# Performance work log

Hardware: AMD Instinct MI355X
Metric: run time of the kernel (lower is better)

## Reference

```python
import jax, jax.numpy as jnp
import numpy as np

NTOKEN, NINP, NHID = 50257, 256, 256
B, T = 64, 2048
RES, FC1 = 10, NHID // 3
EPS = 1e-5

def lrelu(x, p=0.01):
    return jnp.maximum(x, x * p)

def setup_inputs() -> dict:
    key = jax.random.key(0)
    ks = jax.random.split(key, 12)
    s = 0.05
    inp = {
        "input": jax.random.randint(ks[0], (B, T), 0, NTOKEN),
        "hx": jnp.zeros((B, NHID), jnp.float32),
        "cx": jnp.zeros((B, NHID), jnp.float32),
        "seq_len": jax.random.randint(ks[1], (B,), 1, T + 1),  # lengths in [1, T]
        "emb_w": jax.random.uniform(ks[2], (NTOKEN, NINP), jnp.float32, -0.1, 0.1),
        "W_ih": jax.random.normal(ks[3], (4 * NHID, NINP), jnp.float32) * s,
        "W_hh": jax.random.normal(ks[4], (4 * NHID, NHID), jnp.float32) * s,
        "b_ih": jnp.zeros((4 * NHID,), jnp.float32),
        "b_hh": jnp.zeros((4 * NHID,), jnp.float32),
        "rfc1_w": jax.random.normal(ks[5], (RES, NHID), jnp.float32) * s,
        "rfc1_b": jnp.zeros((RES,), jnp.float32),
        "rbn_g": jnp.ones((RES,), jnp.float32),
        "rbn_b": jnp.zeros((RES,), jnp.float32),
        "rbn_rm": jnp.zeros((RES,), jnp.float32),
        "rbn_rv": jnp.ones((RES,), jnp.float32),
        "rfc2_w": jax.random.normal(ks[6], (NHID, RES), jnp.float32) * s,
        "rfc2_b": jnp.zeros((NHID,), jnp.float32),
        "fc1_w": jax.random.normal(ks[7], (FC1, NHID), jnp.float32) * s,
        "fc1_b": jnp.zeros((FC1,), jnp.float32),
        "bn1_g": jnp.ones((FC1,), jnp.float32),
        "bn1_b": jnp.zeros((FC1,), jnp.float32),
        "bn1_rm": jnp.zeros((FC1,), jnp.float32),
        "bn1_rv": jnp.ones((FC1,), jnp.float32),
        "fc2_w": jax.random.normal(ks[8], (2, FC1), jnp.float32) * s,
        "fc2_b": jnp.zeros((2,), jnp.float32),
    }
    return inp

def reference(input, hx, cx, seq_len, emb_w, W_ih, W_hh, b_ih, b_hh,
              rfc1_w, rfc1_b, rbn_g, rbn_b, rbn_rm, rbn_rv, rfc2_w, rfc2_b,
              fc1_w, fc1_b, bn1_g, bn1_b, bn1_rm, bn1_rv, fc2_w, fc2_b):
    # eval mode: dropout = identity, noise = 0, BatchNorm uses running stats
    emb = emb_w[input.T]  # [T, B, ninp]
    # precompute input-side gates once (batched matmul) -> [T, B, 4*nhid]
    x_gates = jnp.einsum('tbi,gi->tbg', emb, W_ih) + b_ih + b_hh

    def step(carry, xg):
        h, c = carry
        gates = xg + h @ W_hh.T
        i, f, g, o = jnp.split(gates, 4, axis=-1)
        c = jax.nn.sigmoid(f) * c + jax.nn.sigmoid(i) * jnp.tanh(g)
        h = jax.nn.sigmoid(o) * jnp.tanh(c)
        return (h, c), h

    (hx_f, cx_f), outs = jax.lax.scan(step, (hx, cx), x_gates)  # outs: [T, B, nhid]

    # ragged mean pooling over first seq_len[b] steps
    mask = (jnp.arange(T)[:, None] < seq_len[None, :]).astype(outs.dtype)  # [T, B]
    feature = jnp.einsum('tbh,tb->bh', outs, mask) / seq_len[:, None].astype(outs.dtype)

    # ResNet block (eval)
    res = jax.nn.relu(feature) @ rfc1_w.T + rfc1_b
    res = jax.nn.relu(res)
    res = (res - rbn_rm) * jax.lax.rsqrt(rbn_rv + EPS) * rbn_g + rbn_b
    feature = feature + res @ rfc2_w.T + rfc2_b

    # classifier head
    fc = feature @ fc1_w.T + fc1_b
    fc = (fc - bn1_rm) * jax.lax.rsqrt(bn1_rv + EPS) * bn1_g + bn1_b
    fc = lrelu(fc)
    logits = fc @ fc2_w.T + fc2_b
    logp = jax.nn.log_softmax(logits, axis=-1)
    return (logp, hx_f, cx_f)
```

## Files before the change

kernel.cpp:

```cpp
#include <hip/hip_runtime.h>
#include <cstdint>


#define NTOKEN 50257
#define NINP 256
#define NHID 256
#define BB 64
#define TT 2048
#define NRES 10
#define NFC1 85
#define EPSV 1e-5f

#define NREGF 45
#define NLDSF 19

typedef _Float16 f16;
typedef _Float16 f16x2 __attribute__((ext_vector_type(2)));
typedef _Float16 f16x4 __attribute__((ext_vector_type(4)));
typedef _Float16 f16x8 __attribute__((ext_vector_type(8)));
typedef float f32x4 __attribute__((ext_vector_type(4)));

static __device__ __forceinline__ float sigm(float x) { return 1.0f / (1.0f + __expf(-x)); }
static __device__ __forceinline__ float tanh_(float x) {
  float ax = fabsf(x);
  float e = __expf(-2.0f * ax);
  float t = (1.0f - e) / (1.0f + e);
  return x < 0.0f ? -t : t;
}

__global__ void k0_convert(const float* __restrict__ emb_w, const float* __restrict__ W_ih,
                           const float* __restrict__ b_ih, const float* __restrict__ b_hh,
                           f16* __restrict__ emb16, f16* __restrict__ wih16,
                           float* __restrict__ bias) {
  int64_t i = (int64_t)blockIdx.x * blockDim.x + threadIdx.x;
  if (i < (int64_t)NTOKEN * NINP) emb16[i] = (f16)emb_w[i];
  if (i < 4 * NHID * NINP) wih16[i] = (f16)W_ih[i];
  if (i < 4 * NHID) bias[i] = b_ih[i] + b_hh[i];
}

__global__ void k0b_whh(const float* __restrict__ Whh, f16* __restrict__ whh16) {
  int i = blockIdx.x * 256 + threadIdx.x;
  if (i < 4 * NHID * NHID) whh16[i] = (f16)Whh[i];
}

__global__ __launch_bounds__(256) void k1_gemm(const f16* __restrict__ emb16,
                                               const f16* __restrict__ wih16,
                                               const float* __restrict__ bias,
                                               f16* __restrict__ xgtab) {
  __shared__ __align__(16) f16 a_lds[64][40];
  __shared__ __align__(16) f16 b_lds[256][40];
  const int mt = blockIdx.x;
  const int nt0 = blockIdx.y * 256;
  const int tid = threadIdx.x;
  const int lane = tid & 63;
  const int w = tid >> 6;
  const int quad = lane >> 4;
  const int l16 = lane & 15;

  f32x4 acc[16];
#pragma unroll
  for (int i = 0; i < 16; i++) acc[i] = (f32x4){0.f, 0.f, 0.f, 0.f};

  const int ar = tid >> 2;
  int av = mt * 64 + ar;
  if (av > NTOKEN - 1) av = NTOKEN - 1;
  const int ac = (tid & 3) * 8;

  for (int kb = 0; kb < 256; kb += 32) {
    *(uint4*)&a_lds[ar][ac] = *(const uint4*)&emb16[av * 256 + kb + ac];
    {
      const uint4* bs = (const uint4*)&wih16[(nt0 + tid) * 256 + kb];
      uint4* bd = (uint4*)&b_lds[tid][0];
      bd[0] = bs[0]; bd[1] = bs[1]; bd[2] = bs[2]; bd[3] = bs[3];
    }
    __syncthreads();
    f16x8 af = *(const f16x8*)&a_lds[w * 16 + l16][quad * 8];
#pragma unroll
    for (int nt = 0; nt < 16; nt++) {
      f16x8 bf = *(const f16x8*)&b_lds[nt * 16 + l16][quad * 8];
      acc[nt] = __builtin_amdgcn_mfma_f32_16x16x32_f16(af, bf, acc[nt], 0, 0, 0);
    }
    __syncthreads();
  }
#pragma unroll
  for (int nt = 0; nt < 16; nt++) {
#pragma unroll
    for (int rg = 0; rg < 4; rg++) {
      int v = mt * 64 + w * 16 + quad * 4 + rg;
      if (v < NTOKEN) {
        int n = nt0 + nt * 16 + l16;
        xgtab[v * 1024 + nt * 64 + l16 * 4 + blockIdx.y] = (f16)(acc[nt][rg] + bias[n]);
      }
    }
  }
}

__global__ __attribute__((amdgpu_flat_work_group_size(512, 512), amdgpu_waves_per_eu(2, 2)))
void k2_rnn(const int* __restrict__ input, const float* __restrict__ hx0,
            const float* __restrict__ cx0, const int* __restrict__ seq_len,
            const f16* __restrict__ whh16, const f16* __restrict__ xgtab,
            float* __restrict__ feat, float* __restrict__ out_hx,
            float* __restrict__ out_cx) {
  __shared__ __align__(16) f16 wlds[8][NLDSF][64][8];
  __shared__ __align__(16) f16 hbuf[2][256];

  const int b = blockIdx.x;
  const int tid = threadIdx.x;
  const int w = tid >> 6;
  const int lane = tid & 63;
  const int quad = lane >> 4;
  const int l16 = lane & 15;

  const int goff = (w * 32 + l16) * 256 + quad * 8;

  f16x8 wreg[NREGF];
#pragma unroll
  for (int ks = 0; ks < 8; ++ks) {
#pragma unroll
    for (int nt = 0; nt < 8; ++nt) {
      const int f = ks * 8 + nt;
      const int g = nt >> 1, hh = nt & 1;
      f16x8 fr = *(const f16x8*)(whh16 + (g * 256 + hh * 16) * 256 + ks * 32 + goff);
      if (f < NREGF) wreg[f] = fr;
      else *(f16x8*)&wlds[w][f - NREGF][lane][0] = fr;
    }
  }
#pragma unroll
  for (int f = 0; f < NREGF; ++f) {
    asm volatile("" : "+v"(wreg[f]));
  }

  float cst[2] = {0.f, 0.f}, pool2[2] = {0.f, 0.f}, hlast[2] = {0.f, 0.f};
  if (quad == 0) {
#pragma unroll
    for (int hh = 0; hh < 2; ++hh) {
      const int n = w * 32 + hh * 16 + l16;
      hbuf[0][n] = (f16)hx0[b * 256 + n];
      cst[hh] = cx0[b * 256 + n];
    }
  }
  const int L = seq_len[b];
  const int* tokp = input + b * TT;
  int tok_cur = tokp[0];
  __syncthreads();

#pragma unroll 1
  for (int t = 0; t < TT; ++t) {
    const int cur = t & 1;

    uint2 xg0 = {0u, 0u}, xg1 = {0u, 0u};
    if (quad == 0) {
      const f16* xr = xgtab + (int64_t)tok_cur * 1024 + w * 128 + l16 * 4;
      xg0 = *(const uint2*)xr;
      xg1 = *(const uint2*)(xr + 64);
    }
    const int tok_nx = tokp[(t + 1 < TT) ? (t + 1) : (TT - 1)];

    f32x4 acc[8];
#pragma unroll
    for (int nt = 0; nt < 8; ++nt) acc[nt] = (f32x4){0.f, 0.f, 0.f, 0.f};

#pragma unroll
    for (int ks = 0; ks < 8; ++ks) {
      f16x8 af;
#pragma unroll
      for (int z = 0; z < 8; ++z) af[z] = (f16)0;
      if (l16 == 0) af = *(const f16x8*)&hbuf[cur][ks * 32 + quad * 8];
#pragma unroll
      for (int nt = 0; nt < 8; ++nt) {
        const int f = ks * 8 + nt;
        f16x8 bf;
        if (f < NREGF) bf = wreg[f];
        else bf = *(const f16x8*)&wlds[w][f - NREGF][lane][0];
        acc[nt] = __builtin_amdgcn_mfma_f32_16x16x32_f16(af, bf, acc[nt], 0, 0, 0);
      }
    }

    if (quad == 0) {
      const f16x4 xa = __builtin_bit_cast(f16x4, xg0);
      const f16x4 xb = __builtin_bit_cast(f16x4, xg1);
#pragma unroll
      for (int hh = 0; hh < 2; ++hh) {
        const f16x4 xv = hh ? xb : xa;
        const float iv = sigm(acc[0 + hh][0] + (float)xv[0]);
        const float fv = sigm(acc[2 + hh][0] + (float)xv[1]);
        const float gv = tanh_(acc[4 + hh][0] + (float)xv[2]);
        const float ov = sigm(acc[6 + hh][0] + (float)xv[3]);
        const float cc = fv * cst[hh] + iv * gv;
        cst[hh] = cc;
        const float hv = ov * tanh_(cc);
        hlast[hh] = hv;
        if (t < L) pool2[hh] += hv;
        hbuf[cur ^ 1][w * 32 + hh * 16 + l16] = (f16)hv;
      }
    }
    tok_cur = tok_nx;
    __syncthreads();
  }

  if (quad == 0) {
#pragma unroll
    for (int hh = 0; hh < 2; ++hh) {
      const int n = w * 32 + hh * 16 + l16;
      feat[b * 256 + n] = pool2[hh] / (float)L;
      out_hx[b * 256 + n] = hlast[hh];
      out_cx[b * 256 + n] = cst[hh];
    }
  }
}

__global__ __launch_bounds__(256) void k3_head(const float* __restrict__ feat,
    const float* __restrict__ rfc1_w, const float* __restrict__ rfc1_b,
    const float* __restrict__ rbn_g, const float* __restrict__ rbn_b,
    const float* __restrict__ rbn_rm, const float* __restrict__ rbn_rv,
    const float* __restrict__ rfc2_w, const float* __restrict__ rfc2_b,
    const float* __restrict__ fc1_w, const float* __restrict__ fc1_b,
    const float* __restrict__ bn1_g, const float* __restrict__ bn1_b,
    const float* __restrict__ bn1_rm, const float* __restrict__ bn1_rv,
    const float* __restrict__ fc2_w, const float* __restrict__ fc2_b,
    float* __restrict__ logp) {
  __shared__ float f[256];
  __shared__ float f2[256];
  __shared__ float res[16];
  __shared__ float fcv[96];
  const int b = blockIdx.x, tid = threadIdx.x;
  const int wv = tid >> 6, lane = tid & 63;
  f[tid] = feat[b * 256 + tid];
  __syncthreads();
  for (int r = wv; r < NRES; r += 4) {
    float p = 0.f;
#pragma unroll
    for (int j0 = 0; j0 < 4; j0++) {
      int j = lane * 4 + j0;
      p += fmaxf(f[j], 0.f) * rfc1_w[r * 256 + j];
    }
    for (int off = 32; off > 0; off >>= 1) p += __shfl_down(p, off);
    if (lane == 0) {
      float x = p + rfc1_b[r];
      x = fmaxf(x, 0.f);
      x = (x - rbn_rm[r]) * rsqrtf(rbn_rv[r] + EPSV) * rbn_g[r] + rbn_b[r];
      res[r] = x;
    }
  }
  __syncthreads();
  {
    float s = rfc2_b[tid];
#pragma unroll
    for (int r = 0; r < NRES; r++) s += res[r] * rfc2_w[tid * NRES + r];
    f2[tid] = f[tid] + s;
  }
  __syncthreads();
  for (int o = wv; o < NFC1; o += 4) {
    float p = 0.f;
#pragma unroll
    for (int j0 = 0; j0 < 4; j0++) {
      int j = lane * 4 + j0;
      p += f2[j] * fc1_w[o * 256 + j];
    }
    for (int off = 32; off > 0; off >>= 1) p += __shfl_down(p, off);
    if (lane == 0) {
      float x = p + fc1_b[o];
      x = (x - bn1_rm[o]) * rsqrtf(bn1_rv[o] + EPSV) * bn1_g[o] + bn1_b[o];
      x = fmaxf(x, 0.01f * x);
      fcv[o] = x;
    }
  }
  __syncthreads();
  if (tid == 0) {
    float l0 = fc2_b[0], l1 = fc2_b[1];
    for (int o2 = 0; o2 < NFC1; o2++) {
      l0 += fcv[o2] * fc2_w[o2];
      l1 += fcv[o2] * fc2_w[NFC1 + o2];
    }
    float mx = fmaxf(l0, l1);
    float lse = mx + __logf(__expf(l0 - mx) + __expf(l1 - mx));
    logp[b * 2 + 0] = l0 - lse;
    logp[b * 2 + 1] = l1 - lse;
  }
}

extern "C" void kernel_launch(void* const* d_in, const int* in_sizes, int n_in,
                              void* d_out, int out_size, void* d_ws, size_t ws_size,
                              hipStream_t stream) {
  const int*   input  = (const int*)  d_in[0];
  const float* hx     = (const float*)d_in[1];
  const float* cx     = (const float*)d_in[2];
  const int*   seqlen = (const int*)  d_in[3];
  const float* emb_w  = (const float*)d_in[4];
  const float* W_ih   = (const float*)d_in[5];
  const float* W_hh   = (const float*)d_in[6];
  const float* b_ih   = (const float*)d_in[7];
  const float* b_hh   = (const float*)d_in[8];
  const float* rfc1_w = (const float*)d_in[9];
  const float* rfc1_b = (const float*)d_in[10];
  const float* rbn_g  = (const float*)d_in[11];
  const float* rbn_b  = (const float*)d_in[12];
  const float* rbn_rm = (const float*)d_in[13];
  const float* rbn_rv = (const float*)d_in[14];
  const float* rfc2_w = (const float*)d_in[15];
  const float* rfc2_b = (const float*)d_in[16];
  const float* fc1_w  = (const float*)d_in[17];
  const float* fc1_b  = (const float*)d_in[18];
  const float* bn1_g  = (const float*)d_in[19];
  const float* bn1_b  = (const float*)d_in[20];
  const float* bn1_rm = (const float*)d_in[21];
  const float* bn1_rv = (const float*)d_in[22];
  const float* fc2_w  = (const float*)d_in[23];
  const float* fc2_b  = (const float*)d_in[24];

  char* ws = (char*)d_ws;
  f16*   emb16 = (f16*)(ws);
  f16*   whh16 = (f16*)(ws);
  f16*   wih16 = (f16*)(ws + 25731584);
  float* bias  = (float*)(ws + 26255872);
  f16*   xgtab = (f16*)(ws + 26259968);
  float* feat  = (float*)(ws + 129186304);

  float* out = (float*)d_out;

  k0_convert<<<dim3(NTOKEN), 256, 0, stream>>>(emb_w, W_ih, b_ih, b_hh, emb16, wih16, bias);
  k1_gemm<<<dim3((NTOKEN + 63) / 64, 4), 256, 0, stream>>>(emb16, wih16, bias, xgtab);
  k0b_whh<<<dim3((4 * NHID * NHID + 255) / 256), 256, 0, stream>>>(W_hh, whh16);
  k2_rnn<<<dim3(BB), 512, 0, stream>>>(input, hx, cx, seqlen, whh16, xgtab, feat,
                                       out + 128, out + 128 + BB * NHID);
  k3_head<<<dim3(BB), 256, 0, stream>>>(feat, rfc1_w, rfc1_b, rbn_g, rbn_b, rbn_rm, rbn_rv,
                                        rfc2_w, rfc2_b, fc1_w, fc1_b, bn1_g, bn1_b, bn1_rm,
                                        bn1_rv, fc2_w, fc2_b, out);
}
```

Before: 4.790 ms.

## Hold recurrent weights in AGPRs and stream two tiles from global per step

The register-resident W_hh fragments move from VGPRs to AGPRs via inline-asm MFMA, which frees VGPR pressure. Two fragments that no longer fit are reloaded from global memory on every timestep. The A operand is now zeroed once outside the loop instead of being rebuilt per k-step. The aim is to keep all weights on-chip without spills, at the cost of two global loads per step on the serial recurrence path.

```diff
diff --git a/kernel.cpp b/kernel.cpp
--- a/kernel.cpp
+++ b/kernel.cpp
@@ -11,8 +11,9 @@
 #define NFC1 85
 #define EPSV 1e-5f
 
-#define NREGF 45
+#define NREGF 43
 #define NLDSF 19
+#define FSTRM (NREGF + NLDSF)
 
 typedef _Float16 f16;
 typedef _Float16 f16x2 __attribute__((ext_vector_type(2)));
@@ -26,6 +27,13 @@
   float e = __expf(-2.0f * ax);
   float t = (1.0f - e) / (1.0f + e);
   return x < 0.0f ? -t : t;
+}
+
+static __device__ __forceinline__ void mfma_ba(f32x4& c, f16x8 a, const f16x8& b_agpr) {
+  asm("v_mfma_f32_16x16x32_f16 %0, %1, %2, %0" : "+a"(c) : "v"(a), "a"(b_agpr));
+}
+static __device__ __forceinline__ void mfma_bv(f32x4& c, f16x8 a, f16x8 b) {
+  asm("v_mfma_f32_16x16x32_f16 %0, %1, %2, %0" : "+a"(c) : "v"(a), "v"(b));
 }
 
 __global__ void k0_convert(const float* __restrict__ emb_w, const float* __restrict__ W_ih,
@@ -113,22 +121,25 @@
 
   const int goff = (w * 32 + l16) * 256 + quad * 8;
 
-  f16x8 wreg[NREGF];
+  f16x8 wa[NREGF];
 #pragma unroll
   for (int ks = 0; ks < 8; ++ks) {
 #pragma unroll
     for (int nt = 0; nt < 8; ++nt) {
       const int f = ks * 8 + nt;
+      if (f >= FSTRM) continue;
       const int g = nt >> 1, hh = nt & 1;
       f16x8 fr = *(const f16x8*)(whh16 + (g * 256 + hh * 16) * 256 + ks * 32 + goff);
-      if (f < NREGF) wreg[f] = fr;
+      if (f < NREGF) wa[f] = fr;
       else *(f16x8*)&wlds[w][f - NREGF][lane][0] = fr;
     }
   }
 #pragma unroll
   for (int f = 0; f < NREGF; ++f) {
-    asm volatile("" : "+v"(wreg[f]));
-  }
+    asm volatile("" : "+a"(wa[f]));
+  }
+  const f16* sp62 = whh16 + (3 * 256 + 0 * 16) * 256 + 7 * 32 + goff;
+  const f16* sp63 = whh16 + (3 * 256 + 1 * 16) * 256 + 7 * 32 + goff;
 
   float cst[2] = {0.f, 0.f}, pool2[2] = {0.f, 0.f}, hlast[2] = {0.f, 0.f};
   if (quad == 0) {
@@ -142,11 +153,16 @@
   const int L = seq_len[b];
   const int* tokp = input + b * TT;
   int tok_cur = tokp[0];
+
+  f16x8 af = {};
   __syncthreads();
 
 #pragma unroll 1
   for (int t = 0; t < TT; ++t) {
     const int cur = t & 1;
+
+    f16x8 s62 = *(const f16x8*)sp62;
+    f16x8 s63 = *(const f16x8*)sp63;
 
     uint2 xg0 = {0u, 0u}, xg1 = {0u, 0u};
     if (quad == 0) {
@@ -162,17 +178,18 @@
 
 #pragma unroll
     for (int ks = 0; ks < 8; ++ks) {
-      f16x8 af;
-#pragma unroll
-      for (int z = 0; z < 8; ++z) af[z] = (f16)0;
       if (l16 == 0) af = *(const f16x8*)&hbuf[cur][ks * 32 + quad * 8];
 #pragma unroll
       for (int nt = 0; nt < 8; ++nt) {
         const int f = ks * 8 + nt;
-        f16x8 bf;
-        if (f < NREGF) bf = wreg[f];
-        else bf = *(const f16x8*)&wlds[w][f - NREGF][lane][0];
-        acc[nt] = __builtin_amdgcn_mfma_f32_16x16x32_f16(af, bf, acc[nt], 0, 0, 0);
+        if (f < NREGF) {
+          mfma_ba(acc[nt], af, wa[f]);
+        } else if (f < FSTRM) {
+          f16x8 bf = *(const f16x8*)&wlds[w][f - NREGF][lane][0];
+          mfma_bv(acc[nt], af, bf);
+        } else {
+          mfma_bv(acc[nt], af, (f == 62) ? s62 : s63);
+        }
       }
     }
 
```

Result: slower. 5.117 ms (+6.8%).

## Keep all W_hh fragments in AGPRs and prefetch gate inputs one step ahead

Applied to the files above, without the earlier changes.

Moves all 64 recurrent-weight MFMA fragments into accumulator registers (AGPRs) via an asm constraint, replacing the previous split between VGPRs and LDS. This removes the per-step LDS reads for 19 weight fragments on the sequential critical path. It also software-pipelines the input-gate table lookup so step t+1's gate values are loaded while step t computes, hiding global-memory latency. The cost is higher register pressure, 256 AGPR dwords per lane, which may cause spills or copies if the compiler cannot feed MFMA B operands directly from AGPRs.

```diff
diff --git a/kernel.cpp b/kernel.cpp
--- a/kernel.cpp
+++ b/kernel.cpp
@@ -10,9 +10,6 @@
 #define NRES 10
 #define NFC1 85
 #define EPSV 1e-5f
-
-#define NREGF 45
-#define NLDSF 19
 
 typedef _Float16 f16;
 typedef _Float16 f16x2 __attribute__((ext_vector_type(2)));
@@ -101,7 +98,6 @@
             const f16* __restrict__ whh16, const f16* __restrict__ xgtab,
             float* __restrict__ feat, float* __restrict__ out_hx,
             float* __restrict__ out_cx) {
-  __shared__ __align__(16) f16 wlds[8][NLDSF][64][8];
   __shared__ __align__(16) f16 hbuf[2][256];
 
   const int b = blockIdx.x;
@@ -113,21 +109,19 @@
 
   const int goff = (w * 32 + l16) * 256 + quad * 8;
 
-  f16x8 wreg[NREGF];
+  f16x8 wa[64];
 #pragma unroll
   for (int ks = 0; ks < 8; ++ks) {
 #pragma unroll
     for (int nt = 0; nt < 8; ++nt) {
-      const int f = ks * 8 + nt;
       const int g = nt >> 1, hh = nt & 1;
-      f16x8 fr = *(const f16x8*)(whh16 + (g * 256 + hh * 16) * 256 + ks * 32 + goff);
-      if (f < NREGF) wreg[f] = fr;
-      else *(f16x8*)&wlds[w][f - NREGF][lane][0] = fr;
-    }
-  }
-#pragma unroll
-  for (int f = 0; f < NREGF; ++f) {
-    asm volatile("" : "+v"(wreg[f]));
+      wa[ks * 8 + nt] =
+          *(const f16x8*)(whh16 + (g * 256 + hh * 16) * 256 + ks * 32 + goff);
+    }
+  }
+#pragma unroll
+  for (int f = 0; f < 64; ++f) {
+    asm volatile("" : "+a"(wa[f]));
   }
 
   float cst[2] = {0.f, 0.f}, pool2[2] = {0.f, 0.f}, hlast[2] = {0.f, 0.f};
@@ -141,20 +135,27 @@
   }
   const int L = seq_len[b];
   const int* tokp = input + b * TT;
-  int tok_cur = tokp[0];
+
+  int tok_nx = tokp[1];
+  uint2 xgc0 = {0u, 0u}, xgc1 = {0u, 0u};
+  if (quad == 0) {
+    const f16* xr = xgtab + (int64_t)tokp[0] * 1024 + w * 128 + l16 * 4;
+    xgc0 = *(const uint2*)xr;
+    xgc1 = *(const uint2*)(xr + 64);
+  }
   __syncthreads();
 
 #pragma unroll 1
   for (int t = 0; t < TT; ++t) {
     const int cur = t & 1;
 
-    uint2 xg0 = {0u, 0u}, xg1 = {0u, 0u};
+    uint2 xgn0 = {0u, 0u}, xgn1 = {0u, 0u};
     if (quad == 0) {
-      const f16* xr = xgtab + (int64_t)tok_cur * 1024 + w * 128 + l16 * 4;
-      xg0 = *(const uint2*)xr;
-      xg1 = *(const uint2*)(xr + 64);
-    }
-    const int tok_nx = tokp[(t + 1 < TT) ? (t + 1) : (TT - 1)];
+      const f16* xr = xgtab + (int64_t)tok_nx * 1024 + w * 128 + l16 * 4;
+      xgn0 = *(const uint2*)xr;
+      xgn1 = *(const uint2*)(xr + 64);
+    }
+    const int tok_n2 = tokp[(t + 2 < TT) ? (t + 2) : (TT - 1)];
 
     f32x4 acc[8];
 #pragma unroll
@@ -168,17 +169,14 @@
       if (l16 == 0) af = *(const f16x8*)&hbuf[cur][ks * 32 + quad * 8];
 #pragma unroll
       for (int nt = 0; nt < 8; ++nt) {
-        const int f = ks * 8 + nt;
-        f16x8 bf;
-        if (f < NREGF) bf = wreg[f];
-        else bf = *(const f16x8*)&wlds[w][f - NREGF][lane][0];
-        acc[nt] = __builtin_amdgcn_mfma_f32_16x16x32_f16(af, bf, acc[nt], 0, 0, 0);
+        acc[nt] = __builtin_amdgcn_mfma_f32_16x16x32_f16(af, wa[ks * 8 + nt],
+                                                         acc[nt], 0, 0, 0);
       }
     }
 
     if (quad == 0) {
-      const f16x4 xa = __builtin_bit_cast(f16x4, xg0);
-      const f16x4 xb = __builtin_bit_cast(f16x4, xg1);
+      const f16x4 xa = __builtin_bit_cast(f16x4, xgc0);
+      const f16x4 xb = __builtin_bit_cast(f16x4, xgc1);
 #pragma unroll
       for (int hh = 0; hh < 2; ++hh) {
         const f16x4 xv = hh ? xb : xa;
@@ -194,7 +192,8 @@
         hbuf[cur ^ 1][w * 32 + hh * 16 + l16] = (f16)hv;
       }
     }
-    tok_cur = tok_nx;
+    xgc0 = xgn0; xgc1 = xgn1;
+    tok_nx = tok_n2;
     __syncthreads();
   }
 
```

Measured after the change: 12.31 ms. 157% more time.
